# Optimization experiments

Hardware: AMD Instinct MI355X
Metric: run time of the kernel (lower is better)

The kernel has to match this reference:

```python
import jax, jax.numpy as jnp
import numpy as np

N = 50000      # nodes
E = 1600000    # edges (avg degree 32)
D = 64         # d_node
DE = 32        # d_edge
H = 4          # heads
L = 3          # layers


def _ln(x, g, b):
    mu = x.mean(-1, keepdims=True)
    var = ((x - mu) ** 2).mean(-1, keepdims=True)
    return (x - mu) / jnp.sqrt(var + 1e-5) * g + b


def setup_inputs() -> dict:
    key = jax.random.key(0)
    ks = jax.random.split(key, 16)
    s = 0.05
    return {
        "node_features": jax.random.normal(ks[0], (N, D), jnp.float32),
        "edge_features": jax.random.normal(ks[1], (E, DE), jnp.float32),
        "edge_index": jax.random.randint(ks[2], (2, E), 0, N),
        "Wq": jax.random.normal(ks[3], (L, D, D), jnp.float32) * s,
        "Wk": jax.random.normal(ks[4], (L, D, D), jnp.float32) * s,
        "Wv": jax.random.normal(ks[5], (L, D, D), jnp.float32) * s,
        "Wo": jax.random.normal(ks[6], (L, D, D), jnp.float32) * s,
        "We": jax.random.normal(ks[7], (L, DE, H), jnp.float32) * s,   # edge-conditioned score bias
        "Wem": jax.random.normal(ks[8], (L, 2 * D + DE, DE), jnp.float32) * s,
        "bem": jnp.zeros((L, DE), jnp.float32),
        "gn": jnp.ones((L, D), jnp.float32),
        "bn": jnp.zeros((L, D), jnp.float32),
        "ge": jnp.ones((L, DE), jnp.float32),
        "be": jnp.zeros((L, DE), jnp.float32),
    }


def _delta_forward(h, e, src, dst, Wq, Wk, Wv, Wo, We, Wem, bem, gn, bn, ge, be):
    n = h.shape[0]
    dh = D // H
    for i in range(L):
        # --- node attention over edges (sparse, per-dst segment softmax) ---
        q = (h @ Wq[i]).reshape(n, H, dh)
        k = (h @ Wk[i]).reshape(n, H, dh)
        v = (h @ Wv[i]).reshape(n, H, dh)
        scores = jnp.einsum('ehd,ehd->eh', q[dst], k[src]) / jnp.sqrt(jnp.float32(dh))
        scores = scores + e @ We[i]                         # edge-conditioned bias [E,H]
        m = jax.ops.segment_max(scores, dst, num_segments=n)
        p = jnp.exp(scores - m[dst])
        denom = jax.ops.segment_sum(p, dst, num_segments=n)
        alpha = p / (denom[dst] + 1e-9)                      # [E,H]
        msg = (alpha[:, :, None] * v[src]).reshape(-1, D)    # [E,D]
        agg = jax.ops.segment_sum(msg, dst, num_segments=n)  # [N,D]
        h = _ln(h + agg @ Wo[i], gn[i], bn[i])
        # --- edge update conditioned on endpoint nodes ---
        emsg = jax.nn.gelu(jnp.concatenate([h[src], h[dst], e], axis=-1) @ Wem[i] + bem[i])
        e = _ln(e + emsg, ge[i], be[i])
    return h


def reference(node_features, edge_features, edge_index, Wq, Wk, Wv, Wo, We, Wem, bem, gn, bn, ge, be):
    src = edge_index[0]
    dst = edge_index[1]
    return _delta_forward(node_features, edge_features, src, dst,
                          Wq, Wk, Wv, Wo, We, Wem, bem, gn, bn, ge, be)
```

## Files before the change

kernel.cpp:

```cpp
#include <hip/hip_runtime.h>
#include <hip/hip_bf16.h>
#include <math.h>

#define NN 50000
#define NE 1600000
#define D 64
#define DE 32
#define H 4
#define DH 16
#define L 3

typedef __attribute__((ext_vector_type(8))) short bf16x8;
typedef __attribute__((ext_vector_type(8))) short s16x8;
typedef __attribute__((ext_vector_type(4))) float f32x4;

__device__ __forceinline__ short f2b(float f) {
    __hip_bfloat16 h = __float2bfloat16(f);
    short s;
    __builtin_memcpy(&s, &h, 2);
    return s;
}
__device__ __forceinline__ float b2f(unsigned short u) {
    unsigned int x = ((unsigned int)u) << 16;
    float f; __builtin_memcpy(&f, &x, 4); return f;
}
__device__ __forceinline__ float b2f_lo(unsigned int p) {
    unsigned int x = p << 16;
    float f; __builtin_memcpy(&f, &x, 4); return f;
}
__device__ __forceinline__ float b2f_hi(unsigned int p) {
    unsigned int x = p & 0xffff0000u;
    float f; __builtin_memcpy(&f, &x, 4); return f;
}


__global__ void deg_kernel(const int* __restrict__ dst, int* __restrict__ cnt) {
    int e = blockIdx.x * 256 + threadIdx.x;
    if (e >= NE) return;
    atomicAdd(&cnt[dst[e]], 1);
}

__global__ void block_sum_kernel(const int* __restrict__ cnt, int* __restrict__ bsum) {
    int b = blockIdx.x, t = threadIdx.x;
    int base = b * 1024 + t * 4;
    int s = 0;
#pragma unroll
    for (int i = 0; i < 4; i++) { int idx = base + i; if (idx < NN) s += cnt[idx]; }
#pragma unroll
    for (int off = 32; off; off >>= 1) s += __shfl_down(s, off);
    __shared__ int wsum[4];
    if ((t & 63) == 0) wsum[t >> 6] = s;
    __syncthreads();
    if (t == 0) bsum[b] = wsum[0] + wsum[1] + wsum[2] + wsum[3];
}

__global__ void scan_bsum_kernel(int* __restrict__ bsum, int nb) {
    int t = threadIdx.x;
    int v = (t < nb) ? bsum[t] : 0;
    int x = v;
#pragma unroll
    for (int off = 1; off < 64; off <<= 1) {
        int y = __shfl_up(x, off);
        if (t >= off) x += y;
    }
    if (t < nb) bsum[t] = x - v;
}

__global__ void scan_block_kernel(const int* __restrict__ cnt, const int* __restrict__ bsum,
                                  int* __restrict__ offsets) {
    int b = blockIdx.x, t = threadIdx.x;
    int base = b * 1024 + t * 4;
    int v[4]; int s = 0;
#pragma unroll
    for (int i = 0; i < 4; i++) { int idx = base + i; v[i] = (idx < NN) ? cnt[idx] : 0; s += v[i]; }
    int lane = t & 63, w = t >> 6;
    int x = s;
#pragma unroll
    for (int off = 1; off < 64; off <<= 1) {
        int y = __shfl_up(x, off);
        if (lane >= off) x += y;
    }
    __shared__ int wsum[4];
    if (lane == 63) wsum[w] = x;
    __syncthreads();
    int woff = 0;
    for (int i = 0; i < w; i++) woff += wsum[i];
    int run = bsum[b] + woff + x - s;
#pragma unroll
    for (int i = 0; i < 4; i++) {
        int idx = base + i;
        if (idx < NN) offsets[idx] = run;
        run += v[i];
    }
}

__global__ void scatter_kernel(const int* __restrict__ dst,
                               const int* __restrict__ offsets,
                               int* __restrict__ cursor,
                               int* __restrict__ sorted_eid) {
    int e = blockIdx.x * 256 + threadIdx.x;
    if (e >= NE) return;
    int d0 = dst[e];
    int pos = atomicAdd(&cursor[d0], 1);
    sorted_eid[offsets[d0] + pos] = e;
}

__global__ void eperm_kernel(const float* __restrict__ e32, const int* __restrict__ sorted_eid,
                             const int* __restrict__ src, const int* __restrict__ dst,
                             const float* __restrict__ We0,
                             unsigned short* __restrict__ eb_s,
                             float* __restrict__ ebias_s,
                             int* __restrict__ sorted_src,
                             int* __restrict__ sorted_dst) {
    int t = blockIdx.x * 256 + threadIdx.x;
    if (t >= NE * 4) return;
    int p = t >> 2;
    int c = (t & 3) * 8;
    int eid = sorted_eid[p];
    const float* ep = e32 + (size_t)eid * DE + c;
    float4 x0 = *(const float4*)(ep);
    float4 x1 = *(const float4*)(ep + 4);
    float e8[8] = {x0.x, x0.y, x0.z, x0.w, x1.x, x1.y, x1.z, x1.w};
    s16x8 ob;
#pragma unroll
    for (int i = 0; i < 8; i++) ob[i] = f2b(e8[i]);
    *(s16x8*)(eb_s + (size_t)p * DE + c) = ob;
    float p0 = 0.f, p1 = 0.f, p2 = 0.f, p3 = 0.f;
#pragma unroll
    for (int i = 0; i < 8; i++) {
        float4 w = *(const float4*)(We0 + (c + i) * 4);
        p0 += e8[i] * w.x; p1 += e8[i] * w.y; p2 += e8[i] * w.z; p3 += e8[i] * w.w;
    }
#pragma unroll
    for (int off = 1; off < 4; off <<= 1) {
        p0 += __shfl_xor(p0, off, 4);
        p1 += __shfl_xor(p1, off, 4);
        p2 += __shfl_xor(p2, off, 4);
        p3 += __shfl_xor(p3, off, 4);
    }
    if ((t & 3) == 0) {
        float4 o; o.x = p0; o.y = p1; o.z = p2; o.w = p3;
        *(float4*)(ebias_s + (size_t)p * H) = o;
        sorted_src[p] = src[eid];
        sorted_dst[p] = dst[eid];
    }
}

__global__ void wconv_kernel(const float* __restrict__ Wem, unsigned short* __restrict__ Wt) {
    int t = blockIdx.x * 256 + threadIdx.x;
    if (t >= L * 32 * 160) return;
    int l = t / 5120;
    int r = t % 5120;
    int n = r / 160;
    int k = r % 160;
    Wt[t] = (unsigned short)f2b(Wem[l * 5120 + k * 32 + n]);
}

__global__ void wsplit_kernel(const float* __restrict__ Wq, const float* __restrict__ Wk,
                              const float* __restrict__ Wv, const float* __restrict__ Wo,
                              unsigned short* __restrict__ WT_hi,
                              unsigned short* __restrict__ WT_lo) {
    int t = blockIdx.x * 256 + threadIdx.x;
    if (t >= L * 4 * 64 * 64) return;
    int k = t & 63;
    int n = (t >> 6) & 63;
    int mat = (t >> 12) & 3;
    int l = t >> 14;
    const float* W = (mat == 0) ? Wq : (mat == 1) ? Wk : (mat == 2) ? Wv : Wo;
    float w = W[l * 4096 + k * 64 + n];
    unsigned short hi = (unsigned short)f2b(w);
    float lo = w - b2f(hi);
    WT_hi[t] = hi;
    WT_lo[t] = (unsigned short)f2b(lo);
}

__global__ void hconv_kernel(const float* __restrict__ nf, float* __restrict__ h,
                             unsigned short* __restrict__ hb) {
    int t = blockIdx.x * 256 + threadIdx.x;
    if (t >= NN * D) return;
    float x = nf[t];
    h[t] = x;
    hb[t] = (unsigned short)f2b(x);
}


__global__ __launch_bounds__(256, 8)
void qkv_kernel(const float* __restrict__ h,
                const unsigned short* __restrict__ WT_hi,
                const unsigned short* __restrict__ WT_lo,
                float* __restrict__ q, unsigned int* __restrict__ kv) {
    int lane = threadIdx.x & 63;
    int wv = threadIdx.x >> 6;
    int m = lane & 15, quad = lane >> 4;
    int base = blockIdx.x * 16;

    const float* hp = h + (size_t)(base + m) * D + quad * 8;
    float af[16];
    *(f32x4*)&af[0]  = *(const f32x4*)(hp);
    *(f32x4*)&af[4]  = *(const f32x4*)(hp + 4);
    *(f32x4*)&af[8]  = *(const f32x4*)(hp + 32);
    *(f32x4*)&af[12] = *(const f32x4*)(hp + 36);
    bf16x8 a0h, a0l, a1h, a1l;
#pragma unroll
    for (int j = 0; j < 8; j++) {
        short h0 = f2b(af[j]);
        short h1 = f2b(af[8 + j]);
        a0h[j] = h0; a0l[j] = f2b(af[j] - b2f((unsigned short)h0));
        a1h[j] = h1; a1l[j] = f2b(af[8 + j] - b2f((unsigned short)h1));
    }

    f32x4 acc[3];
#pragma unroll
    for (int mat = 0; mat < 3; mat++) {
        const unsigned short* bh = WT_hi + ((size_t)mat * 64 + wv * 16 + m) * 64 + quad * 8;
        const unsigned short* bl = WT_lo + ((size_t)mat * 64 + wv * 16 + m) * 64 + quad * 8;
        bf16x8 bh0 = *(const bf16x8*)(bh);
        bf16x8 bh1 = *(const bf16x8*)(bh + 32);
        bf16x8 bl0 = *(const bf16x8*)(bl);
        bf16x8 bl1 = *(const bf16x8*)(bl + 32);
        f32x4 c = {0.f, 0.f, 0.f, 0.f};
        c = __builtin_amdgcn_mfma_f32_16x16x32_bf16(a0h, bh0, c, 0, 0, 0);
        c = __builtin_amdgcn_mfma_f32_16x16x32_bf16(a1h, bh1, c, 0, 0, 0);
        c = __builtin_amdgcn_mfma_f32_16x16x32_bf16(a0h, bl0, c, 0, 0, 0);
        c = __builtin_amdgcn_mfma_f32_16x16x32_bf16(a1h, bl1, c, 0, 0, 0);
        c = __builtin_amdgcn_mfma_f32_16x16x32_bf16(a0l, bh0, c, 0, 0, 0);
        c = __builtin_amdgcn_mfma_f32_16x16x32_bf16(a1l, bh1, c, 0, 0, 0);
        acc[mat] = c;
    }

#pragma unroll
    for (int reg = 0; reg < 4; reg++) {
        int row = base + quad * 4 + reg;
        int col = wv * 16 + m;
        q[(size_t)row * D + col] = acc[0][reg] * 0.25f;
        unsigned int kb = (unsigned short)f2b(acc[1][reg]);
        unsigned int vb = (unsigned short)f2b(acc[2][reg]);
        kv[(size_t)row * D + col] = (vb << 16) | kb;
    }
}

__global__ void attn_kernel(const float* __restrict__ q, const unsigned int* __restrict__ kv,
                            const float* __restrict__ ebias_s,
                            const int* __restrict__ sorted_src,
                            const int* __restrict__ offsets,
                            float* __restrict__ agg) {
    int node = blockIdx.x * 4 + threadIdx.y;
    node = __builtin_amdgcn_readfirstlane(node);
    if (node >= NN) return;
    int lane = threadIdx.x;
    int hh = lane >> 4;
    float qv = q[node * D + lane];
    int beg = offsets[node];
    int end = (node == NN - 1) ? NE : offsets[node + 1];
    float mmax = -INFINITY, den = 0.f, acc = 0.f;
    int i = beg;
    for (; i + 8 <= end; i += 8) {
        int ss[8]; unsigned int kk8[8]; float bb8[8], dd[8];
#pragma unroll
        for (int u = 0; u < 8; u++) ss[u] = sorted_src[i + u];
#pragma unroll
        for (int u = 0; u < 8; u++) kk8[u] = kv[ss[u] * D + lane];
#pragma unroll
        for (int u = 0; u < 8; u++) bb8[u] = ebias_s[(i + u) * H + hh];
#pragma unroll
        for (int u = 0; u < 8; u++) dd[u] = qv * b2f_lo(kk8[u]);
#pragma unroll
        for (int off = 1; off < 16; off <<= 1) {
#pragma unroll
            for (int u = 0; u < 8; u++) dd[u] += __shfl_xor(dd[u], off, 16);
        }
        float nm = mmax;
#pragma unroll
        for (int u = 0; u < 8; u++) { dd[u] += bb8[u]; nm = fmaxf(nm, dd[u]); }
        float scale = __expf(mmax - nm);
        float ps = 0.f, av = 0.f;
#pragma unroll
        for (int u = 0; u < 8; u++) {
            float p = __expf(dd[u] - nm);
            ps += p;
            av += p * b2f_hi(kk8[u]);
        }
        den = den * scale + ps;
        acc = acc * scale + av;
        mmax = nm;
    }
    for (; i < end; i++) {
        int s = sorted_src[i];
        unsigned int kvv = kv[s * D + lane];
        float b = ebias_s[i * H + hh];
        float dot = qv * b2f_lo(kvv);
#pragma unroll
        for (int off = 1; off < 16; off <<= 1) dot += __shfl_xor(dot, off, 16);
        float score = dot + b;
        float nm = fmaxf(mmax, score);
        float scale = __expf(mmax - nm);
        float p = __expf(score - nm);
        den = den * scale + p;
        acc = acc * scale + p * b2f_hi(kvv);
        mmax = nm;
    }
    agg[node * D + lane] = acc / (den + 1e-9f);
}

__global__ __launch_bounds__(256, 8)
void node_update_kernel(float* __restrict__ h, const float* __restrict__ agg,
                        const unsigned short* __restrict__ WoT_hi,
                        const unsigned short* __restrict__ WoT_lo,
                        const float* __restrict__ gn,
                        const float* __restrict__ bn,
                        unsigned short* __restrict__ hb) {
    __shared__ float sx[16][68];
    int lane = threadIdx.x & 63;
    int wv = threadIdx.x >> 6;
    int m = lane & 15, quad = lane >> 4;
    int base = blockIdx.x * 16;

    const float* ap = agg + (size_t)(base + m) * D + quad * 8;
    float af[16];
    *(f32x4*)&af[0]  = *(const f32x4*)(ap);
    *(f32x4*)&af[4]  = *(const f32x4*)(ap + 4);
    *(f32x4*)&af[8]  = *(const f32x4*)(ap + 32);
    *(f32x4*)&af[12] = *(const f32x4*)(ap + 36);
    bf16x8 a0h, a0l, a1h, a1l;
#pragma unroll
    for (int j = 0; j < 8; j++) {
        short h0 = f2b(af[j]);
        short h1 = f2b(af[8 + j]);
        a0h[j] = h0; a0l[j] = f2b(af[j] - b2f((unsigned short)h0));
        a1h[j] = h1; a1l[j] = f2b(af[8 + j] - b2f((unsigned short)h1));
    }
    const unsigned short* bh = WoT_hi + ((size_t)wv * 16 + m) * 64 + quad * 8;
    const unsigned short* bl = WoT_lo + ((size_t)wv * 16 + m) * 64 + quad * 8;
    bf16x8 bh0 = *(const bf16x8*)(bh);
    bf16x8 bh1 = *(const bf16x8*)(bh + 32);
    bf16x8 bl0 = *(const bf16x8*)(bl);
    bf16x8 bl1 = *(const bf16x8*)(bl + 32);
    f32x4 c = {0.f, 0.f, 0.f, 0.f};
    c = __builtin_amdgcn_mfma_f32_16x16x32_bf16(a0h, bh0, c, 0, 0, 0);
    c = __builtin_amdgcn_mfma_f32_16x16x32_bf16(a1h, bh1, c, 0, 0, 0);
    c = __builtin_amdgcn_mfma_f32_16x16x32_bf16(a0h, bl0, c, 0, 0, 0);
    c = __builtin_amdgcn_mfma_f32_16x16x32_bf16(a1h, bl1, c, 0, 0, 0);
    c = __builtin_amdgcn_mfma_f32_16x16x32_bf16(a0l, bh0, c, 0, 0, 0);
    c = __builtin_amdgcn_mfma_f32_16x16x32_bf16(a1l, bh1, c, 0, 0, 0);

#pragma unroll
    for (int reg = 0; reg < 4; reg++) {
        int row = quad * 4 + reg;
        int col = wv * 16 + m;
        sx[row][col] = c[reg] + h[(size_t)(base + row) * D + col];
    }
    __syncthreads();

    float gcol = gn[lane], bcol = bn[lane];
#pragma unroll
    for (int it = 0; it < 4; it++) {
        int ln = wv * 4 + it;
        int node = base + ln;
        float x = sx[ln][lane];
        float sum = x, sq = x * x;
#pragma unroll
        for (int off = 32; off; off >>= 1) {
            sum += __shfl_xor(sum, off);
            sq += __shfl_xor(sq, off);
        }
        float mu = sum * (1.f / 64.f);
        float var = sq * (1.f / 64.f) - mu * mu;
        float out = (x - mu) * rsqrtf(var + 1e-5f) * gcol + bcol;
        h[(size_t)node * D + lane] = out;
        hb[(size_t)node * D + lane] = (unsigned short)f2b(out);
    }
}

__global__ __launch_bounds__(256, 4)
void edge_update_mfma_kernel(const unsigned short* __restrict__ hb,
                             unsigned short* __restrict__ eb_s,
                             const int* __restrict__ sorted_src,
                             const int* __restrict__ sorted_dst,
                             const unsigned short* __restrict__ Wt,
                             const float* __restrict__ bem,
                             const float* __restrict__ ge,
                             const float* __restrict__ be,
                             const float* __restrict__ We_next,
                             float* __restrict__ ebias_s,
                             int do_bias, int do_estore) {
    __shared__ __align__(16) float ytr[4][16][36];
    int tid = threadIdx.x;
    int wave = tid >> 6;
    int lane = tid & 63;
    int wbase = blockIdx.x * 256 + wave * 64;
    int m = lane & 15;
    int quad = lane >> 4;

    const unsigned short* w0 = Wt + m * 160 + quad * 8;
    const unsigned short* w1 = Wt + (m + 16) * 160 + quad * 8;
    bf16x8 B0[5], B1[5];
#pragma unroll
    for (int ks = 0; ks < 5; ks++) {
        B0[ks] = *(const bf16x8*)(w0 + ks * 32);
        B1[ks] = *(const bf16x8*)(w1 + ks * 32);
    }
    bf16x8 wb;
#pragma unroll
    for (int j = 0; j < 8; j++) {
        float w = (do_bias && m < 4) ? We_next[(quad * 8 + j) * 4 + m] : 0.f;
        wb[j] = f2b(w);
    }
    float bm0 = bem[m], bm1 = bem[m + 16];
    float4 g0v = *(const float4*)(ge + quad * 8);
    float4 g1v = *(const float4*)(ge + quad * 8 + 4);
    float4 b0v = *(const float4*)(be + quad * 8);
    float4 b1v = *(const float4*)(be + quad * 8 + 4);
    float gg[8] = {g0v.x, g0v.y, g0v.z, g0v.w, g1v.x, g1v.y, g1v.z, g1v.w};
    float bbv[8] = {b0v.x, b0v.y, b0v.z, b0v.w, b1v.x, b1v.y, b1v.z, b1v.w};

    for (int g = 0; g < 4; g++) {
        int we = wbase + g * 16;
        int p_m = we + m;
        int s_idx = sorted_src[p_m], d_idx = sorted_dst[p_m];
        const unsigned short* as = hb + (size_t)s_idx * D + quad * 8;
        const unsigned short* ad = hb + (size_t)d_idx * D + quad * 8;
        bf16x8 a_s0 = *(const bf16x8*)(as);
        bf16x8 a_s1 = *(const bf16x8*)(as + 32);
        bf16x8 a_d0 = *(const bf16x8*)(ad);
        bf16x8 a_d1 = *(const bf16x8*)(ad + 32);
        bf16x8 ea = *(const bf16x8*)(eb_s + (size_t)p_m * DE + quad * 8);

        f32x4 c0 = {0.f, 0.f, 0.f, 0.f};
        f32x4 c1 = {0.f, 0.f, 0.f, 0.f};
#pragma unroll
        for (int ks = 0; ks < 4; ks++) {
            bf16x8 a = (ks == 0) ? a_s0 : (ks == 1) ? a_s1 : (ks == 2) ? a_d0 : a_d1;
            c0 = __builtin_amdgcn_mfma_f32_16x16x32_bf16(a, B0[ks], c0, 0, 0, 0);
            c1 = __builtin_amdgcn_mfma_f32_16x16x32_bf16(a, B1[ks], c1, 0, 0, 0);
        }
        c0 = __builtin_amdgcn_mfma_f32_16x16x32_bf16(ea, B0[4], c0, 0, 0, 0);
        c1 = __builtin_amdgcn_mfma_f32_16x16x32_bf16(ea, B1[4], c1, 0, 0, 0);

#pragma unroll
        for (int reg = 0; reg < 4; reg++) {
            int row = quad * 4 + reg;
            float y0 = c0[reg] + bm0;
            float y1 = c1[reg] + bm1;
            float u0 = 1.5957691216057308f * (y0 + 0.044715f * y0 * y0 * y0);
            float u1 = 1.5957691216057308f * (y1 + 0.044715f * y1 * y1 * y1);
            float t0 = 1.f - 2.f / (1.f + __expf(u0));
            float t1 = 1.f - 2.f / (1.f + __expf(u1));
            ytr[wave][row][m] = 0.5f * y0 * (1.f + t0);
            ytr[wave][row][m + 16] = 0.5f * y1 * (1.f + t1);
        }

        float y[8];
        *(f32x4*)&y[0] = *(const f32x4*)&ytr[wave][m][quad * 8];
        *(f32x4*)&y[4] = *(const f32x4*)&ytr[wave][m][quad * 8 + 4];
        float s = 0.f, sq = 0.f;
#pragma unroll
        for (int j = 0; j < 8; j++) {
            y[j] += b2f((unsigned short)ea[j]);
            s += y[j];
            sq += y[j] * y[j];
        }
        s += __shfl_xor(s, 16); s += __shfl_xor(s, 32);
        sq += __shfl_xor(sq, 16); sq += __shfl_xor(sq, 32);
        float mu = s * (1.f / 32.f);
        float var = sq * (1.f / 32.f) - mu * mu;
        float inv = rsqrtf(var + 1e-5f);

        bf16x8 zb;
#pragma unroll
        for (int j = 0; j < 8; j++) {
            float z = (y[j] - mu) * inv * gg[j] + bbv[j];
            zb[j] = f2b(z);
        }
        if (do_estore) {
            *(s16x8*)(eb_s + (size_t)p_m * DE + quad * 8) = zb;
        }
        if (do_bias) {
            f32x4 db = {0.f, 0.f, 0.f, 0.f};
            db = __builtin_amdgcn_mfma_f32_16x16x32_bf16(zb, wb, db, 0, 0, 0);
            if (m < 4) {
#pragma unroll
                for (int reg = 0; reg < 4; reg++) {
                    ebias_s[(we + quad * 4 + reg) * H + m] = db[reg];
                }
            }
        }
    }
}

extern "C" void kernel_launch(void* const* d_in, const int* in_sizes, int n_in,
                              void* d_out, int out_size, void* d_ws, size_t ws_size,
                              hipStream_t stream) {
    const float* node_features = (const float*)d_in[0];
    const float* e = (const float*)d_in[1];
    const int* edge_index = (const int*)d_in[2];
    const int* src = edge_index;
    const int* dst = edge_index + NE;
    const float* Wq = (const float*)d_in[3];
    const float* Wk = (const float*)d_in[4];
    const float* Wv = (const float*)d_in[5];
    const float* Wo = (const float*)d_in[6];
    const float* We = (const float*)d_in[7];
    const float* Wem = (const float*)d_in[8];
    const float* bem = (const float*)d_in[9];
    const float* gn = (const float*)d_in[10];
    const float* bn = (const float*)d_in[11];
    const float* ge = (const float*)d_in[12];
    const float* be = (const float*)d_in[13];

    float* h = (float*)d_out;

    float* ws = (float*)d_ws;
    float* q = ws;
    unsigned int* kv = (unsigned int*)(q + NN * D);
    float* agg = (float*)(kv + NN * D);
    float* ebias_s = agg + NN * D;
    int* offsets = (int*)(ebias_s + (size_t)NE * H);
    int* cursor = offsets + NN;
    int* bsum = cursor + NN;
    int* sorted_eid = bsum + 64;
    int* sorted_src = sorted_eid + NE;
    int* sorted_dst = sorted_src + NE;
    unsigned short* Wt = (unsigned short*)(sorted_dst + NE);
    unsigned short* hb = Wt + L * 32 * 160;
    unsigned short* eb_s = hb + NN * D;
    unsigned short* WT_hi = eb_s + (size_t)NE * DE;
    unsigned short* WT_lo = WT_hi + L * 4 * 64 * 64;

    const int NB = (NN + 1023) / 1024;

    hipMemsetAsync(cursor, 0, NN * sizeof(int), stream);
    deg_kernel<<<(NE + 255) / 256, 256, 0, stream>>>(dst, cursor);
    block_sum_kernel<<<NB, 256, 0, stream>>>(cursor, bsum);
    scan_bsum_kernel<<<1, 64, 0, stream>>>(bsum, NB);
    scan_block_kernel<<<NB, 256, 0, stream>>>(cursor, bsum, offsets);
    hipMemsetAsync(cursor, 0, NN * sizeof(int), stream);
    scatter_kernel<<<(NE + 255) / 256, 256, 0, stream>>>(dst, offsets, cursor, sorted_eid);
    eperm_kernel<<<(NE * 4 + 255) / 256, 256, 0, stream>>>(e, sorted_eid, src, dst, We,
                                                           eb_s, ebias_s,
                                                           sorted_src, sorted_dst);
    wconv_kernel<<<(L * 32 * 160 + 255) / 256, 256, 0, stream>>>(Wem, Wt);
    wsplit_kernel<<<(L * 4 * 64 * 64 + 255) / 256, 256, 0, stream>>>(Wq, Wk, Wv, Wo,
                                                                     WT_hi, WT_lo);
    hconv_kernel<<<(NN * D + 255) / 256, 256, 0, stream>>>(node_features, h, hb);

    for (int layer = 0; layer < L; layer++) {
        const unsigned short* WT_hi_l = WT_hi + (size_t)layer * 4 * 4096;
        const unsigned short* WT_lo_l = WT_lo + (size_t)layer * 4 * 4096;
        const unsigned short* Wt_l = Wt + layer * 32 * 160;
        const float* bem_l = bem + layer * DE;
        const float* gn_l = gn + layer * D;
        const float* bn_l = bn + layer * D;
        const float* ge_l = ge + layer * DE;
        const float* be_l = be + layer * DE;

        qkv_kernel<<<NN / 16, 256, 0, stream>>>(h, WT_hi_l, WT_lo_l, q, kv);
        attn_kernel<<<NN / 4, dim3(64, 4), 0, stream>>>(q, kv, ebias_s, sorted_src,
                                                        offsets, agg);
        node_update_kernel<<<NN / 16, 256, 0, stream>>>(h, agg,
                                                        WT_hi_l + 3 * 4096,
                                                        WT_lo_l + 3 * 4096,
                                                        gn_l, bn_l, hb);
        if (layer < L - 1) {
            const float* We_next = We + (layer + 1) * DE * H;
            edge_update_mfma_kernel<<<NE / 256, 256, 0, stream>>>(hb, eb_s, sorted_src,
                                                                  sorted_dst, Wt_l,
                                                                  bem_l, ge_l, be_l,
                                                                  We_next, ebias_s,
                                                                  1, layer == 0 ? 1 : 0);
        }
    }
}
```

Measured before the change: 1.135 ms.

## Rework attention to edge-per-lane gathers and streamline CSR construction

The attention kernel now assigns one edge per lane within each 16-lane head group. Each lane loads its 16 packed K/V values with vector loads, computes the full dot product locally and accumulates p·V in registers. Per-head partial sums are then reduced through shared memory. This drops the 16-way shuffle reduction per edge and the online max rescaling, which means exp is taken without subtracting the segment max, an overflow risk if scores grow large. Separately, the CSR build writes the scan result into the cursor array so the scatter places edges directly, packs edge id and source into an int2, and fills sorted_dst with a per-node kernel. This removes a memset and the separate gathers of src/dst in the permutation kernel.

```diff
diff --git a/kernel.cpp b/kernel.cpp
--- a/kernel.cpp
+++ b/kernel.cpp
@@ -13,6 +13,7 @@
 typedef __attribute__((ext_vector_type(8))) short bf16x8;
 typedef __attribute__((ext_vector_type(8))) short s16x8;
 typedef __attribute__((ext_vector_type(4))) float f32x4;
+typedef __attribute__((ext_vector_type(4))) unsigned int u32x4;
 
 __device__ __forceinline__ short f2b(float f) {
     __hip_bfloat16 h = __float2bfloat16(f);
@@ -66,7 +67,7 @@
     if (t < nb) bsum[t] = x - v;
 }
 
-__global__ void scan_block_kernel(const int* __restrict__ cnt, const int* __restrict__ bsum,
+__global__ void scan_block_kernel(int* __restrict__ cnt, const int* __restrict__ bsum,
                                   int* __restrict__ offsets) {
     int b = blockIdx.x, t = threadIdx.x;
     int base = b * 1024 + t * 4;
@@ -89,34 +90,39 @@
 #pragma unroll
     for (int i = 0; i < 4; i++) {
         int idx = base + i;
-        if (idx < NN) offsets[idx] = run;
+        if (idx < NN) { offsets[idx] = run; cnt[idx] = run; }
         run += v[i];
     }
 }
 
-__global__ void scatter_kernel(const int* __restrict__ dst,
-                               const int* __restrict__ offsets,
+__global__ void scatter_kernel(const int* __restrict__ src, const int* __restrict__ dst,
                                int* __restrict__ cursor,
-                               int* __restrict__ sorted_eid) {
+                               int2* __restrict__ sorted_es) {
     int e = blockIdx.x * 256 + threadIdx.x;
     if (e >= NE) return;
     int d0 = dst[e];
     int pos = atomicAdd(&cursor[d0], 1);
-    sorted_eid[offsets[d0] + pos] = e;
-}
-
-__global__ void eperm_kernel(const float* __restrict__ e32, const int* __restrict__ sorted_eid,
-                             const int* __restrict__ src, const int* __restrict__ dst,
+    int2 v; v.x = e; v.y = src[e];
+    sorted_es[pos] = v;
+}
+
+__global__ void fill_dst_kernel(const int* __restrict__ offsets, int* __restrict__ sorted_dst) {
+    int n = blockIdx.x * 256 + threadIdx.x;
+    if (n >= NN) return;
+    int b = offsets[n];
+    int e = (n == NN - 1) ? NE : offsets[n + 1];
+    for (int i = b; i < e; i++) sorted_dst[i] = n;
+}
+
+__global__ void eperm_kernel(const float* __restrict__ e32, const int2* __restrict__ sorted_es,
                              const float* __restrict__ We0,
                              unsigned short* __restrict__ eb_s,
-                             float* __restrict__ ebias_s,
-                             int* __restrict__ sorted_src,
-                             int* __restrict__ sorted_dst) {
+                             float* __restrict__ ebias_s) {
     int t = blockIdx.x * 256 + threadIdx.x;
     if (t >= NE * 4) return;
     int p = t >> 2;
     int c = (t & 3) * 8;
-    int eid = sorted_eid[p];
+    int eid = sorted_es[p].x;
     const float* ep = e32 + (size_t)eid * DE + c;
     float4 x0 = *(const float4*)(ep);
     float4 x1 = *(const float4*)(ep + 4);
@@ -141,8 +147,6 @@
     if ((t & 3) == 0) {
         float4 o; o.x = p0; o.y = p1; o.z = p2; o.w = p3;
         *(float4*)(ebias_s + (size_t)p * H) = o;
-        sorted_src[p] = src[eid];
-        sorted_dst[p] = dst[eid];
     }
 }
 
@@ -239,67 +243,65 @@
     }
 }
 
-__global__ void attn_kernel(const float* __restrict__ q, const unsigned int* __restrict__ kv,
-                            const float* __restrict__ ebias_s,
-                            const int* __restrict__ sorted_src,
-                            const int* __restrict__ offsets,
-                            float* __restrict__ agg) {
-    int node = blockIdx.x * 4 + threadIdx.y;
+__global__ __launch_bounds__(256, 8)
+void attn_kernel(const float* __restrict__ q, const unsigned int* __restrict__ kv,
+                 const float* __restrict__ ebias_s,
+                 const int2* __restrict__ es,
+                 const int* __restrict__ offsets,
+                 float* __restrict__ agg) {
+    __shared__ __align__(16) float sacc[4][4][16][20];
+    int wave = threadIdx.y;
+    int node = blockIdx.x * 4 + wave;
     node = __builtin_amdgcn_readfirstlane(node);
     if (node >= NN) return;
     int lane = threadIdx.x;
-    int hh = lane >> 4;
-    float qv = q[node * D + lane];
+    int u = lane & 15, hh = lane >> 4;
+
+    float qv[16];
+    const float* qp = q + (size_t)node * D + hh * 16;
+    *(f32x4*)&qv[0]  = *(const f32x4*)(qp);
+    *(f32x4*)&qv[4]  = *(const f32x4*)(qp + 4);
+    *(f32x4*)&qv[8]  = *(const f32x4*)(qp + 8);
+    *(f32x4*)&qv[12] = *(const f32x4*)(qp + 12);
+
     int beg = offsets[node];
     int end = (node == NN - 1) ? NE : offsets[node + 1];
-    float mmax = -INFINITY, den = 0.f, acc = 0.f;
-    int i = beg;
-    for (; i + 8 <= end; i += 8) {
-        int ss[8]; unsigned int kk8[8]; float bb8[8], dd[8];
-#pragma unroll
-        for (int u = 0; u < 8; u++) ss[u] = sorted_src[i + u];
-#pragma unroll
-        for (int u = 0; u < 8; u++) kk8[u] = kv[ss[u] * D + lane];
-#pragma unroll
-        for (int u = 0; u < 8; u++) bb8[u] = ebias_s[(i + u) * H + hh];
-#pragma unroll
-        for (int u = 0; u < 8; u++) dd[u] = qv * b2f_lo(kk8[u]);
-#pragma unroll
-        for (int off = 1; off < 16; off <<= 1) {
-#pragma unroll
-            for (int u = 0; u < 8; u++) dd[u] += __shfl_xor(dd[u], off, 16);
-        }
-        float nm = mmax;
-#pragma unroll
-        for (int u = 0; u < 8; u++) { dd[u] += bb8[u]; nm = fmaxf(nm, dd[u]); }
-        float scale = __expf(mmax - nm);
-        float ps = 0.f, av = 0.f;
-#pragma unroll
-        for (int u = 0; u < 8; u++) {
-            float p = __expf(dd[u] - nm);
-            ps += p;
-            av += p * b2f_hi(kk8[u]);
-        }
-        den = den * scale + ps;
-        acc = acc * scale + av;
-        mmax = nm;
-    }
-    for (; i < end; i++) {
-        int s = sorted_src[i];
-        unsigned int kvv = kv[s * D + lane];
-        float b = ebias_s[i * H + hh];
-        float dot = qv * b2f_lo(kvv);
-#pragma unroll
-        for (int off = 1; off < 16; off <<= 1) dot += __shfl_xor(dot, off, 16);
-        float score = dot + b;
-        float nm = fmaxf(mmax, score);
-        float scale = __expf(mmax - nm);
-        float p = __expf(score - nm);
-        den = den * scale + p;
-        acc = acc * scale + p * b2f_hi(kvv);
-        mmax = nm;
-    }
-    agg[node * D + lane] = acc / (den + 1e-9f);
+    float den = 0.f;
+    float acc[16];
+#pragma unroll
+    for (int j = 0; j < 16; j++) acc[j] = 0.f;
+
+    for (int i = beg; i < end; i += 16) {
+        int idx = i + u;
+        bool valid = idx < end;
+        int sidx = valid ? idx : (end - 1);
+        int s = es[sidx].y;
+        float bias = ebias_s[sidx * H + hh];
+        const unsigned int* kp = kv + (size_t)s * D + hh * 16;
+        unsigned int kr[16];
+        *(u32x4*)&kr[0]  = *(const u32x4*)(kp);
+        *(u32x4*)&kr[4]  = *(const u32x4*)(kp + 4);
+        *(u32x4*)&kr[8]  = *(const u32x4*)(kp + 8);
+        *(u32x4*)&kr[12] = *(const u32x4*)(kp + 12);
+        float dot = bias;
+#pragma unroll
+        for (int j = 0; j < 16; j++) dot += qv[j] * b2f_lo(kr[j]);
+        float p = valid ? __expf(dot) : 0.f;
+        den += p;
+#pragma unroll
+        for (int j = 0; j < 16; j++) acc[j] += p * b2f_hi(kr[j]);
+    }
+
+    *(f32x4*)&sacc[wave][hh][u][0]  = *(const f32x4*)&acc[0];
+    *(f32x4*)&sacc[wave][hh][u][4]  = *(const f32x4*)&acc[4];
+    *(f32x4*)&sacc[wave][hh][u][8]  = *(const f32x4*)&acc[8];
+    *(f32x4*)&sacc[wave][hh][u][12] = *(const f32x4*)&acc[12];
+#pragma unroll
+    for (int off = 1; off < 16; off <<= 1) den += __shfl_xor(den, off, 16);
+    float o = 0.f;
+#pragma unroll
+    for (int u2 = 0; u2 < 16; u2++) o += sacc[wave][hh][u2][u];
+    agg[(size_t)node * D + hh * 16 + u] = o / (den + 1e-9f);
 }
 
 __global__ __launch_bounds__(256, 8)
@@ -374,7 +376,7 @@
 __global__ __launch_bounds__(256, 4)
 void edge_update_mfma_kernel(const unsigned short* __restrict__ hb,
                              unsigned short* __restrict__ eb_s,
-                             const int* __restrict__ sorted_src,
+                             const int2* __restrict__ es,
                              const int* __restrict__ sorted_dst,
                              const unsigned short* __restrict__ Wt,
                              const float* __restrict__ bem,
@@ -416,7 +418,7 @@
     for (int g = 0; g < 4; g++) {
         int we = wbase + g * 16;
         int p_m = we + m;
-        int s_idx = sorted_src[p_m], d_idx = sorted_dst[p_m];
+        int s_idx = es[p_m].y, d_idx = sorted_dst[p_m];
         const unsigned short* as = hb + (size_t)s_idx * D + quad * 8;
         const unsigned short* ad = hb + (size_t)d_idx * D + quad * 8;
         bf16x8 a_s0 = *(const bf16x8*)(as);
@@ -517,9 +519,8 @@
     int* offsets = (int*)(ebias_s + (size_t)NE * H);
     int* cursor = offsets + NN;
     int* bsum = cursor + NN;
-    int* sorted_eid = bsum + 64;
-    int* sorted_src = sorted_eid + NE;
-    int* sorted_dst = sorted_src + NE;
+    int2* sorted_es = (int2*)(bsum + 64);
+    int* sorted_dst = (int*)(sorted_es + NE);
     unsigned short* Wt = (unsigned short*)(sorted_dst + NE);
     unsigned short* hb = Wt + L * 32 * 160;
     unsigned short* eb_s = hb + NN * D;
@@ -533,11 +534,9 @@
     block_sum_kernel<<<NB, 256, 0, stream>>>(cursor, bsum);
     scan_bsum_kernel<<<1, 64, 0, stream>>>(bsum, NB);
     scan_block_kernel<<<NB, 256, 0, stream>>>(cursor, bsum, offsets);
-    hipMemsetAsync(cursor, 0, NN * sizeof(int), stream);
-    scatter_kernel<<<(NE + 255) / 256, 256, 0, stream>>>(dst, offsets, cursor, sorted_eid);
-    eperm_kernel<<<(NE * 4 + 255) / 256, 256, 0, stream>>>(e, sorted_eid, src, dst, We,
-                                                           eb_s, ebias_s,
-                                                           sorted_src, sorted_dst);
+    scatter_kernel<<<(NE + 255) / 256, 256, 0, stream>>>(src, dst, cursor, sorted_es);
+    fill_dst_kernel<<<(NN + 255) / 256, 256, 0, stream>>>(offsets, sorted_dst);
+    eperm_kernel<<<(NE * 4 + 255) / 256, 256, 0, stream>>>(e, sorted_es, We, eb_s, ebias_s);
     wconv_kernel<<<(L * 32 * 160 + 255) / 256, 256, 0, stream>>>(Wem, Wt);
     wsplit_kernel<<<(L * 4 * 64 * 64 + 255) / 256, 256, 0, stream>>>(Wq, Wk, Wv, Wo,
                                                                      WT_hi, WT_lo);
@@ -554,7 +553,7 @@
         const float* be_l = be + layer * DE;
 
         qkv_kernel<<<NN / 16, 256, 0, stream>>>(h, WT_hi_l, WT_lo_l, q, kv);
-        attn_kernel<<<NN / 4, dim3(64, 4), 0, stream>>>(q, kv, ebias_s, sorted_src,
+        attn_kernel<<<NN / 4, dim3(64, 4), 0, stream>>>(q, kv, ebias_s, sorted_es,
                                                         offsets, agg);
         node_update_kernel<<<NN / 16, 256, 0, stream>>>(h, agg,
                                                         WT_hi_l + 3 * 4096,
@@ -562,7 +561,7 @@
                                                         gn_l, bn_l, hb);
         if (layer < L - 1) {
             const float* We_next = We + (layer + 1) * DE * H;
-            edge_update_mfma_kernel<<<NE / 256, 256, 0, stream>>>(hb, eb_s, sorted_src,
+            edge_update_mfma_kernel<<<NE / 256, 256, 0, stream>>>(hb, eb_s, sorted_es,
                                                                   sorted_dst, Wt_l,
                                                                   bem_l, ge_l, be_l,
                                                                   We_next, ebias_s,
```

New measurement: 1.113 ms. 2.0% less time.
